# Optimization experiments

Measured on AMD Instinct MI355X. Metric: run time of the kernel, lower is better.

Reference implementation:

```python
import jax, jax.numpy as jnp
import numpy as np

B, C, H, W = 4, 2048, 32, 32
HID, A, G = 512, 9, 20
SCALE = 32.0
POS_T, NEG_T = 0.7, 0.3
W_CONF, W_REG = 1.0, 5.0
EPS = 1e-8


def _anchor_base():
    # gen_anc_centers + gen_anc_base: centers at (i+0.5); anc_w=scale, anc_h=scale*ratio; clipped to feature-map extent
    scales = jnp.array([2.0, 4.0, 6.0])
    ratios = jnp.array([0.5, 1.0, 1.5])
    aw = jnp.repeat(scales, 3)                       # [A]
    ah = (scales[:, None] * ratios[None, :]).reshape(-1)
    xc = (jnp.arange(W) + 0.5)[None, :, None]        # [1,W,1]
    yc = (jnp.arange(H) + 0.5)[:, None, None]        # [H,1,1]
    x1 = jnp.clip(xc - aw / 2, 0.0, W)
    y1 = jnp.clip(yc - ah / 2, 0.0, H)
    x2 = jnp.clip(xc + aw / 2, 0.0, W)
    y2 = jnp.clip(yc + ah / 2, 0.0, H)
    anc = jnp.stack(jnp.broadcast_arrays(x1, y1, x2, y2), axis=-1)  # [H,W,A,4]
    return anc.reshape(-1, 4)                        # [N,4], N = H*W*A


def _conv(x, w, b):
    y = jax.lax.conv_general_dilated(x, w, (1, 1), 'SAME',
                                     dimension_numbers=('NCHW', 'OIHW', 'NCHW'))
    return y + b[None, :, None, None]


def setup_inputs():
    key = jax.random.key(0)
    ks = jax.random.split(key, 8)
    feature_map = jax.random.normal(ks[0], (B, C, H, W), jnp.float32)
    # valid GT boxes in pixel coords of a 1024x1024 image
    ctr = jax.random.uniform(ks[1], (B, G, 2), minval=0.15, maxval=0.85) * 1024.0
    wh = jax.random.uniform(ks[2], (B, G, 2), minval=0.05, maxval=0.30) * 1024.0
    gt_bboxes = jnp.clip(jnp.concatenate([ctr - wh / 2, ctr + wh / 2], -1), 0.0, 1024.0)
    gt_classes = jax.random.randint(ks[3], (B, G), 1, 21)
    f1 = 1.0 / np.sqrt(C * 9)
    f2 = 1.0 / np.sqrt(HID)
    conv1_w = jax.random.uniform(ks[4], (HID, C, 3, 3), jnp.float32, -f1, f1)
    conv1_b = jnp.zeros((HID,), jnp.float32)
    conf_w = jax.random.uniform(ks[5], (A, HID, 1, 1), jnp.float32, -f2, f2)
    conf_b = jnp.zeros((A,), jnp.float32)
    reg_w = jax.random.uniform(ks[6], (A * 4, HID, 1, 1), jnp.float32, -f2, f2)
    reg_b = jnp.zeros((A * 4,), jnp.float32)
    return {"feature_map": feature_map, "gt_bboxes": gt_bboxes, "gt_classes": gt_classes,
            "conv1_w": conv1_w, "conv1_b": conv1_b, "conf_w": conf_w, "conf_b": conf_b,
            "reg_w": reg_w, "reg_b": reg_b}


def reference(feature_map, gt_bboxes, gt_classes, conv1_w, conv1_b, conf_w, conf_b, reg_w, reg_b):
    # ProposalModule (dropout = eval identity)
    hid = jax.nn.relu(_conv(feature_map, conv1_w, conv1_b))
    conf = _conv(hid, conf_w, conf_b).transpose(0, 2, 3, 1).reshape(B, -1)       # [B,N]
    offs = _conv(hid, reg_w, reg_b).transpose(0, 2, 3, 1).reshape(B, -1, 4)      # [B,N,4]

    anc = _anchor_base()                              # [N,4]
    gt = gt_bboxes / SCALE                            # project_bboxes p2a

    # IoU [B,N,G]
    lt = jnp.maximum(anc[None, :, None, :2], gt[:, None, :, :2])
    rb = jnp.minimum(anc[None, :, None, 2:], gt[:, None, :, 2:])
    inter = jnp.clip(rb - lt, 0.0).prod(-1)
    area_a = (anc[:, 2] - anc[:, 0]) * (anc[:, 3] - anc[:, 1])
    area_g = (gt[..., 2] - gt[..., 0]) * (gt[..., 3] - gt[..., 1])
    iou = inter / (area_a[None, :, None] + area_g[:, None, :] - inter + EPS)

    # positive: IoU > pos_thresh OR best anchor for each GT; negative: max IoU < neg_thresh
    max_per_gt = iou.max(axis=1, keepdims=True)
    pos = ((iou > POS_T) | ((iou == max_per_gt) & (max_per_gt > EPS))).any(-1)    # [B,N]
    max_per_anc = iou.max(-1)
    gi = iou.argmax(-1)                               # assigned GT per anchor
    neg = (max_per_anc < NEG_T) & (~pos)

    assigned = jnp.take_along_axis(gt, jnp.broadcast_to(gi[:, :, None], gi.shape + (4,)), axis=1)

    acx = (anc[:, 0] + anc[:, 2]) / 2; acy = (anc[:, 1] + anc[:, 3]) / 2
    aw_ = anc[:, 2] - anc[:, 0];       ah_ = anc[:, 3] - anc[:, 1]
    gcx = (assigned[..., 0] + assigned[..., 2]) / 2; gcy = (assigned[..., 1] + assigned[..., 3]) / 2
    gw = assigned[..., 2] - assigned[..., 0];        gh = assigned[..., 3] - assigned[..., 1]
    gt_off = jnp.stack([(gcx - acx) / (aw_ + EPS), (gcy - acy) / (ah_ + EPS),
                        jnp.log((gw + EPS) / (aw_ + EPS)), jnp.log((gh + EPS) / (ah_ + EPS))], -1)

    posf = pos.astype(conf.dtype)
    negf = neg.astype(conf.dtype)
    # BCE-with-logits, reduction='sum' / batch_size (pos target 1, neg target 0)
    cls_loss = ((jax.nn.softplus(-conf) * posf).sum() + (jax.nn.softplus(conf) * negf).sum()) / B
    d = offs - gt_off
    sl1 = jnp.where(jnp.abs(d) < 1.0, 0.5 * d * d, jnp.abs(d) - 0.5)
    reg_loss = (sl1 * posf[..., None]).sum() / B
    total = W_CONF * cls_loss + W_REG * reg_loss

    # generate_proposals from positive anchors + predicted offsets (mask instead of gather for jit)
    pcx = acx + offs[..., 0] * aw_; pcy = acy + offs[..., 1] * ah_
    pw = aw_ * jnp.exp(offs[..., 2]); ph = ah_ * jnp.exp(offs[..., 3])
    proposals = jnp.stack([pcx - pw / 2, pcy - ph / 2, pcx + pw / 2, pcy + ph / 2], -1)
    proposals = proposals * posf[..., None]
    return total, proposals, pos
```

## Files before the change

### kernel.cpp

```cpp
#include <hip/hip_runtime.h>


typedef __bf16 bf16x8 __attribute__((ext_vector_type(8)));
typedef float floatx4 __attribute__((ext_vector_type(4)));

#define NB 4
#define NC 2048
#define NH 32
#define NW 32
#define NHID 512
#define NA 9
#define NG 20
#define NANC 9216
#define NM 4096

#define OFF_XH    0ull
#define OFF_WT    18939904ull
#define OFF_WH    37814272ull
#define OFF_HB    37863424ull
#define OFF_MAXG  37863680ull
#define OFF_SUMS  37864192ull
#define OFF_CTR   37864320ull
#define OFF_HIDP  37864448ull

#define PREP_TX   4096
#define PREP_W    1024
#define PREP_WH   96
#define PREP_HALO 528
#define PREP_MAXG 80
#define PREP_NBLK (PREP_TX + PREP_W + PREP_WH + PREP_HALO + PREP_MAXG + 1)

__device__ __forceinline__ unsigned short f2bf(float f) {
  unsigned int u = __float_as_uint(f);
  u = (u + 0x7fffu + ((u >> 16) & 1u)) >> 16;
  return (unsigned short)u;
}

__device__ __forceinline__ void gload16(const void* g, void* l) {
  __builtin_amdgcn_global_load_lds(
      (const __attribute__((address_space(1))) unsigned int*)g,
      (__attribute__((address_space(3))) unsigned int*)l, 16, 0, 0);
}

__constant__ float c_aw[9] = {2.f,2.f,2.f,4.f,4.f,4.f,6.f,6.f,6.f};
__constant__ float c_ah[9] = {1.f,2.f,3.f,2.f,4.f,6.f,3.f,6.f,9.f};

struct Anc { float x1, y1, x2, y2, areaA; };
__device__ __forceinline__ Anc anc_of(int n) {
  const int a = n % 9, pix = n / 9;
  const int xi = pix & 31, yi = pix >> 5;
  const float hw = c_aw[a]*0.5f, hh = c_ah[a]*0.5f;
  const float xc = xi + 0.5f, yc = yi + 0.5f;
  Anc A;
  A.x1 = fminf(fmaxf(xc - hw, 0.f), 32.f);
  A.y1 = fminf(fmaxf(yc - hh, 0.f), 32.f);
  A.x2 = fminf(fmaxf(xc + hw, 0.f), 32.f);
  A.y2 = fminf(fmaxf(yc + hh, 0.f), 32.f);
  A.areaA = __fmul_rn(__fsub_rn(A.x2, A.x1), __fsub_rn(A.y2, A.y1));
  return A;
}
__device__ __forceinline__ float iou_one(const Anc& A, float4 gp) {
  const float gx1 = gp.x * 0.03125f, gy1 = gp.y * 0.03125f;
  const float gx2 = gp.z * 0.03125f, gy2 = gp.w * 0.03125f;
  const float dx = fmaxf(__fsub_rn(fminf(A.x2, gx2), fmaxf(A.x1, gx1)), 0.f);
  const float dy = fmaxf(__fsub_rn(fminf(A.y2, gy2), fmaxf(A.y1, gy1)), 0.f);
  const float inter = __fmul_rn(dx, dy);
  const float areaG = __fmul_rn(__fsub_rn(gx2, gx1), __fsub_rn(gy2, gy1));
  const float den = __fadd_rn(__fsub_rn(__fadd_rn(A.areaA, areaG), inter), 1e-8f);
  return __fdiv_rn(inter, den);
}

__global__ __launch_bounds__(256) void k_prep(const float* __restrict__ x,
                                              const float* __restrict__ w1,
                                              const float* __restrict__ cw, const float* __restrict__ cb,
                                              const float* __restrict__ rw, const float* __restrict__ rb,
                                              const float* __restrict__ gtb,
                                              unsigned short* __restrict__ xh,
                                              unsigned short* __restrict__ wt,
                                              unsigned short* __restrict__ wh, float* __restrict__ hb,
                                              unsigned int* __restrict__ maxg,
                                              float* __restrict__ sums, unsigned int* __restrict__ ctr) {
  __shared__ float tile[64][33];
  __shared__ unsigned short wlds[9*1024];
  __shared__ float red[4];
  const int bid = blockIdx.x;
  const int tid = threadIdx.x;

  if (bid < PREP_TX) {
    const int c0 = (bid & 31) << 6;
    const int h  = (bid >> 5) & 31;
    const int b  = bid >> 10;
    const float* src = x + (((size_t)b*NC + c0)*NH + h)*NW;
    const int w4 = (tid & 7) << 2, cl = tid >> 3;
#pragma unroll
    for (int j = 0; j < 2; ++j) {
      const int c = cl + j*32;
      const float4 v = *(const float4*)(src + (size_t)c*NH*NW + w4);
      tile[c][w4 + 0] = v.x;
      tile[c][w4 + 1] = v.y;
      tile[c][w4 + 2] = v.z;
      tile[c][w4 + 3] = v.w;
    }
    __syncthreads();
    unsigned short* dst = xh + ((size_t)(b*34 + h + 1)*34 + 1)*2048 + c0;
    const int w2 = tid >> 3, c8 = (tid & 7) << 3;
    unsigned int pk[4];
#pragma unroll
    for (int k = 0; k < 4; ++k) {
      const unsigned int lo = f2bf(tile[c8 + 2*k][w2]);
      const unsigned int hi = f2bf(tile[c8 + 2*k + 1][w2]);
      pk[k] = lo | (hi << 16);
    }
    *(uint4*)(dst + (size_t)w2*2048 + c8) = make_uint4(pk[0], pk[1], pk[2], pk[3]);
    return;
  }
  if (bid < PREP_TX + PREP_W) {
    const int p = bid - PREP_TX;
    const int o = p >> 1, half = p & 1;
    const int c_base = half << 10;
    const float* src = w1 + ((size_t)(o*2048 + c_base))*9;
#pragma unroll
    for (int j = 0; j < 9; ++j) {
      const int f0 = (j*256 + tid)*4;
      const float4 v = *(const float4*)(src + f0);
      const float vv[4] = {v.x, v.y, v.z, v.w};
#pragma unroll
      for (int e = 0; e < 4; ++e) {
        const int f = f0 + e;
        const int c = f/9, g = f - c*9;
        wlds[g*1024 + c] = f2bf(vv[e]);
      }
    }
    __syncthreads();
#pragma unroll
    for (int j = 0; j < 5; ++j) {
      const int idx = j*256 + tid;
      if (idx < 1152) {
        const int g = idx >> 7, off = (idx & 127) << 3;
        *(uint4*)(wt + (size_t)g*NHID*NC + o*2048 + c_base + off) =
            *(const uint4*)(wlds + g*1024 + off);
      }
    }
    return;
  }
  if (bid < PREP_TX + PREP_W + PREP_WH) {
    const int t = (bid - PREP_TX - PREP_W)*256 + tid;
    const int n = t >> 9, c = t & 511;
    float v = 0.f;
    if (n < 9) v = cw[n*512 + c];
    else if (n < 45) v = rw[(n-9)*512 + c];
    wh[t] = f2bf(v);
    if (c == 0) {
      float bv = 0.f;
      if (n < 9) bv = cb[n];
      else if (n < 45) bv = rb[n-9];
      hb[n] = bv;
    }
    return;
  }
  if (bid < PREP_TX + PREP_W + PREP_WH + PREP_HALO) {
    const int q = bid - (PREP_TX + PREP_W + PREP_WH);
    const int b = q / 132, hc = q - b*132;
    int hh, ww;
    if (hc < 34)       { hh = 0;        ww = hc; }
    else if (hc < 68)  { hh = 33;       ww = hc - 34; }
    else if (hc < 100) { hh = hc - 67;  ww = 0; }
    else               { hh = hc - 99;  ww = 33; }
    uint4* dst = (uint4*)(xh + ((size_t)((b*34 + hh)*34 + ww))*2048);
    dst[tid] = make_uint4(0u, 0u, 0u, 0u);
    return;
  }
  if (bid < PREP_TX + PREP_W + PREP_WH + PREP_HALO + PREP_MAXG) {
    const int p = bid - (PREP_TX + PREP_W + PREP_WH + PREP_HALO);
    const int b = p / NG, g = p - b*NG;
    const float4 gp = *(const float4*)(gtb + ((size_t)b*NG + g)*4);
    float m = 0.f;
#pragma unroll
    for (int j = 0; j < 36; ++j)
      m = fmaxf(m, iou_one(anc_of(tid + j*256), gp));
#pragma unroll
    for (int o = 32; o > 0; o >>= 1) m = fmaxf(m, __shfl_xor(m, o));
    if ((tid & 63) == 0) red[tid >> 6] = m;
    __syncthreads();
    if (tid == 0)
      maxg[b*NG + g] = __float_as_uint(fmaxf(fmaxf(red[0], red[1]), fmaxf(red[2], red[3])));
    return;
  }
  if (tid < 2) sums[tid] = 0.f;
  else if (tid == 2) *ctr = 0u;
}

__global__ __launch_bounds__(256, 4) void k_conv_gemm(const unsigned short* __restrict__ xh,
                                                      const unsigned short* __restrict__ wt,
                                                      unsigned short* __restrict__ hidp,
                                                      int csplit, int ksh) {
  __shared__ unsigned short As[128*64] __attribute__((aligned(16)));
  __shared__ unsigned short Bs[128*64] __attribute__((aligned(16)));
  const int t = threadIdx.x;
  const int L = blockIdx.x;
  const int kz = L & ((1 << ksh) - 1);
  const int rem = L >> ksh;
  const int tileM = rem & 31, tileN = rem >> 5;
  const int b = tileM >> 3, h0 = (tileM & 7) << 2;
  const int o0 = tileN << 7;
  const int wv = t >> 6, lane = t & 63;
  const int wm = wv >> 1, wn = wv & 1;
  const int quad = lane >> 4, l16 = lane & 15;
  const int c_base = kz * csplit;

  floatx4 acc[4][4];
#pragma unroll
  for (int mt = 0; mt < 4; ++mt)
#pragma unroll
    for (int nt = 0; nt < 4; ++nt)
      acc[mt][nt] = (floatx4){0.f, 0.f, 0.f, 0.f};

  const int lr = lane >> 3, pos = lane & 7;
  int gA[4], gB[4];
#pragma unroll
  for (int j = 0; j < 4; ++j) {
    const int row = wv*32 + j*8 + lr;
    const int sd = (pos - row) & 7;
    const int hh = h0 + (row >> 5) + 1, ww = (row & 31) + 1;
    gA[j] = ((b*34 + hh)*34 + ww)*2048 + c_base + sd*8;
    gB[j] = (o0 + row)*2048 + c_base + sd*8;
  }

  for (int g = 0; g < 9; ++g) {
    const int dsp = ((g/3 - 1)*34 + (g%3 - 1)) * 2048;
    const unsigned short* wgp = wt + (size_t)g*NHID*NC;
    for (int c0 = 0; c0 < csplit; c0 += 64) {
#pragma unroll
      for (int j = 0; j < 4; ++j) {
        gload16(xh + gA[j] + dsp + c0, As + (wv*32 + j*8)*64);
        gload16(wgp + gB[j] + c0,      Bs + (wv*32 + j*8)*64);
      }
      __syncthreads();
#pragma unroll
      for (int sub = 0; sub < 2; ++sub) {
        const int ps = ((sub*4 + quad) + l16) & 7;
        bf16x8 af[4], bw[4];
#pragma unroll
        for (int mt = 0; mt < 4; ++mt)
          af[mt] = *(const bf16x8*)(As + (wm*64 + mt*16 + l16)*64 + ps*8);
#pragma unroll
        for (int nt = 0; nt < 4; ++nt)
          bw[nt] = *(const bf16x8*)(Bs + (wn*64 + nt*16 + l16)*64 + ps*8);
#pragma unroll
        for (int mt = 0; mt < 4; ++mt)
#pragma unroll
          for (int nt = 0; nt < 4; ++nt)
            acc[mt][nt] = __builtin_amdgcn_mfma_f32_16x16x32_bf16(af[mt], bw[nt], acc[mt][nt], 0, 0, 0);
      }
      __syncthreads();
    }
  }
  unsigned short* hp = hidp + (size_t)kz*NM*NHID;
#pragma unroll
  for (int mt = 0; mt < 4; ++mt) {
    const int m = tileM*128 + wm*64 + mt*16 + quad*4;
#pragma unroll
    for (int nt = 0; nt < 4; ++nt) {
      const int o = o0 + wn*64 + nt*16 + l16;
#pragma unroll
      for (int r = 0; r < 4; ++r)
        hp[(size_t)(m + r)*NHID + o] = f2bf(acc[mt][nt][r]);
    }
  }
}

__device__ __forceinline__ float softplusf(float z) {
  return fmaxf(z, 0.f) + log1pf(expf(-fabsf(z)));
}
__device__ __forceinline__ float sl1f(float d) {
  const float ad = fabsf(d);
  return ad < 1.f ? 0.5f*d*d : ad - 0.5f;
}

__global__ __launch_bounds__(256) void k_heads_assign(const unsigned short* __restrict__ hidp,
                                                      const float* __restrict__ b1,
                                                      const unsigned short* __restrict__ wh,
                                                      const float* __restrict__ hb,
                                                      const float* __restrict__ gtb,
                                                      const unsigned int* __restrict__ maxg,
                                                      float* __restrict__ out,
                                                      float* __restrict__ sums,
                                                      unsigned int* __restrict__ ctr,
                                                      int nsplit) {
  __shared__ float red[4][16][48];
  __shared__ float hl[16][49];
  __shared__ float4 gt_s[20];
  __shared__ float  mg_s[20];
  const int t = threadIdx.x;
  const int bid = blockIdx.x;
  const int b = bid >> 6, pix0 = (bid & 63) << 4;

  if (t < 20) {
    gt_s[t] = *(const float4*)(gtb + ((size_t)b*NG + t)*4);
    mg_s[t] = __uint_as_float(maxg[b*NG + t]);
  }

  const int wv = t >> 6, lane = t & 63;
  const int quad = lane >> 4, l16 = lane & 15;
  floatx4 acc[3];
#pragma unroll
  for (int nt = 0; nt < 3; ++nt) acc[nt] = (floatx4){0.f, 0.f, 0.f, 0.f};

  const int m = bid*16 + l16;
#pragma unroll
  for (int kk = 0; kk < 4; ++kk) {
    const int ch0 = wv*128 + kk*32 + quad*8;
    float s[8] = {0.f,0.f,0.f,0.f,0.f,0.f,0.f,0.f};
    const unsigned short* hp0 = hidp + (size_t)m*NHID + ch0;
#define SP_ACC(SP) do { \
      const uint4 v = *(const uint4*)(hp0 + (size_t)(SP)*NM*NHID); \
      s[0] += __uint_as_float(v.x << 16); s[1] += __uint_as_float(v.x & 0xffff0000u); \
      s[2] += __uint_as_float(v.y << 16); s[3] += __uint_as_float(v.y & 0xffff0000u); \
      s[4] += __uint_as_float(v.z << 16); s[5] += __uint_as_float(v.z & 0xffff0000u); \
      s[6] += __uint_as_float(v.w << 16); s[7] += __uint_as_float(v.w & 0xffff0000u); \
    } while (0)
    if (nsplit == 8) {
#pragma unroll
      for (int sp = 0; sp < 8; ++sp) SP_ACC(sp);
    } else if (nsplit == 4) {
#pragma unroll
      for (int sp = 0; sp < 4; ++sp) SP_ACC(sp);
    } else {
      for (int sp = 0; sp < nsplit; ++sp) SP_ACC(sp);
    }
#undef SP_ACC
    union { unsigned short u[8]; bf16x8 v; } af;
#pragma unroll
    for (int e = 0; e < 8; ++e)
      af.u[e] = f2bf(fmaxf(s[e] + b1[ch0 + e], 0.f));
#pragma unroll
    for (int nt = 0; nt < 3; ++nt) {
      const bf16x8 bf = *(const bf16x8*)(wh + (size_t)(nt*16 + l16)*NHID + ch0);
      acc[nt] = __builtin_amdgcn_mfma_f32_16x16x32_bf16(af.v, bf, acc[nt], 0, 0, 0);
    }
  }
#pragma unroll
  for (int nt = 0; nt < 3; ++nt)
#pragma unroll
    for (int r = 0; r < 4; ++r)
      red[wv][quad*4 + r][nt*16 + l16] = acc[nt][r];
  __syncthreads();
#pragma unroll
  for (int j = 0; j < 3; ++j) {
    const int idx = t + j*256;
    const int i = idx / 48, c = idx - i*48;
    hl[i][c] = red[0][i][c] + red[1][i][c] + red[2][i][c] + red[3][i][c] + hb[c];
  }
  __syncthreads();

  float cs = 0.f, rs = 0.f;
  if (t < 144) {
    const int pixL = t / 9, a = t - pixL*9;
    const int pix = pix0 + pixL;
    const int n = pix*9 + a;
    const int idx = b*NANC + n;
    const Anc A = anc_of(n);

    float mx = -1.f; int gi = 0; bool pos = false;
    for (int g = 0; g < NG; ++g) {
      const float v = iou_one(A, gt_s[g]);
      const float mg = mg_s[g];
      pos = pos || (v > 0.7f) || ((v == mg) && (mg > 1e-8f));
      if (v > mx) { mx = v; gi = g; }
    }
    const bool neg = (mx < 0.3f) && !pos;
    const float posf = pos ? 1.f : 0.f;

    const float conf = hl[pixL][a];
    const float of0 = hl[pixL][9 + a*4 + 0];
    const float of1 = hl[pixL][9 + a*4 + 1];
    const float of2 = hl[pixL][9 + a*4 + 2];
    const float of3 = hl[pixL][9 + a*4 + 3];

    if (pos) cs = softplusf(-conf);
    else if (neg) cs = softplusf(conf);

    const float acx = (A.x1 + A.x2)*0.5f, acy = (A.y1 + A.y2)*0.5f;
    const float aw = A.x2 - A.x1, ah = A.y2 - A.y1;
    if (pos) {
      const float4 gp = gt_s[gi];
      const float gx1 = gp.x*0.03125f, gy1 = gp.y*0.03125f;
      const float gx2 = gp.z*0.03125f, gy2 = gp.w*0.03125f;
      const float gcx = (gx1+gx2)*0.5f, gcy = (gy1+gy2)*0.5f;
      const float gw = gx2-gx1, gh = gy2-gy1;
      const float t0 = (gcx-acx)/(aw+1e-8f), t1 = (gcy-acy)/(ah+1e-8f);
      const float t2 = logf((gw+1e-8f)/(aw+1e-8f)), t3 = logf((gh+1e-8f)/(ah+1e-8f));
      rs = sl1f(of0-t0) + sl1f(of1-t1) + sl1f(of2-t2) + sl1f(of3-t3);
    }

    const float pcx = acx + of0*aw, pcy = acy + of1*ah;
    const float pw = aw*expf(of2), ph = ah*expf(of3);
    float* op = out + 1 + (size_t)idx*4;
    op[0] = (pcx - pw*0.5f)*posf;
    op[1] = (pcy - ph*0.5f)*posf;
    op[2] = (pcx + pw*0.5f)*posf;
    op[3] = (pcy + ph*0.5f)*posf;
    out[1 + 4*(size_t)NB*NANC + idx] = posf;
  }
#pragma unroll
  for (int o = 32; o > 0; o >>= 1) { cs += __shfl_xor(cs, o); rs += __shfl_xor(rs, o); }
  if ((t & 63) == 0) { atomicAdd(&sums[0], cs); atomicAdd(&sums[1], rs); }

  __syncthreads();
  if (t == 0) {
    __threadfence();
    const unsigned int c = atomicAdd(ctr, 1u);
    if (c == 255u) {
      __threadfence();
      const float fcs = atomicAdd(&sums[0], 0.f);
      const float frs = atomicAdd(&sums[1], 0.f);
      out[0] = fcs*0.25f + 5.f*(frs*0.25f);
    }
  }
}

extern "C" void kernel_launch(void* const* d_in, const int* in_sizes, int n_in,
                              void* d_out, int out_size, void* d_ws, size_t ws_size,
                              hipStream_t stream) {
  const float* x   = (const float*)d_in[0];
  const float* gtb = (const float*)d_in[1];
  const float* w1  = (const float*)d_in[3];
  const float* b1  = (const float*)d_in[4];
  const float* cw  = (const float*)d_in[5];
  const float* cb  = (const float*)d_in[6];
  const float* rw  = (const float*)d_in[7];
  const float* rb  = (const float*)d_in[8];
  float* out = (float*)d_out;
  char* ws = (char*)d_ws;

  unsigned short* xh    = (unsigned short*)(ws + OFF_XH);
  unsigned short* wt    = (unsigned short*)(ws + OFF_WT);
  unsigned short* wh    = (unsigned short*)(ws + OFF_WH);
  float*          hb    = (float*)(ws + OFF_HB);
  unsigned int*   maxg  = (unsigned int*)(ws + OFF_MAXG);
  float*          sums  = (float*)(ws + OFF_SUMS);
  unsigned int*   ctr   = (unsigned int*)(ws + OFF_CTR);
  unsigned short* hidp  = (unsigned short*)(ws + OFF_HIDP);

  int nsplit = 8, ksh = 3;
  while (nsplit > 1 && OFF_HIDP + (size_t)nsplit*NM*NHID*2 > ws_size) { nsplit >>= 1; --ksh; }
  const int csplit = NC / nsplit;

  k_prep<<<PREP_NBLK, 256, 0, stream>>>(x, w1, cw, cb, rw, rb, gtb, xh, wt, wh, hb, maxg, sums, ctr);
  k_conv_gemm<<<128*nsplit, 256, 0, stream>>>(xh, wt, hidp, csplit, ksh);
  k_heads_assign<<<256, 256, 0, stream>>>(hidp, b1, wh, hb, gtb, maxg, out, sums, ctr, nsplit);
}
```

Baseline: 225.8 us.

## Pre-swizzle conv weights into MFMA fragment order and load B directly to registers

The weight prep kernel now writes the 3x3 conv weights in a layout matching the MFMA B-fragment order, so each lane in the GEMM loads its bf16x8 fragments straight from global memory. This removes the Bs shared-memory tile and its LDS writes and reads, which frees LDS and may raise occupancy. The cost is that weight tiles shared across blocks are no longer staged through LDS, so each wave issues its own global/L2 loads. Those loads now sit in the K-loop before the barrier.

Result: slower. 250.6 us (+11.0%).

```diff
diff --git a/kernel.cpp b/kernel.cpp
--- a/kernel.cpp
+++ b/kernel.cpp
@@ -118,6 +118,7 @@
     const int p = bid - PREP_TX;
     const int o = p >> 1, half = p & 1;
     const int c_base = half << 10;
+    const int og = o >> 4, l16o = o & 15;
     const float* src = w1 + ((size_t)(o*2048 + c_base))*9;
 #pragma unroll
     for (int j = 0; j < 9; ++j) {
@@ -136,9 +137,12 @@
     for (int j = 0; j < 5; ++j) {
       const int idx = j*256 + tid;
       if (idx < 1152) {
-        const int g = idx >> 7, off = (idx & 127) << 3;
-        *(uint4*)(wt + (size_t)g*NHID*NC + o*2048 + c_base + off) =
-            *(const uint4*)(wlds + g*1024 + off);
+        const int g = idx >> 7, r = idx & 127;
+        const int cq_loc = r >> 3, s = (r >> 2) & 1, quad = r & 3;
+        const int cqg = (half << 4) + cq_loc;
+        const size_t dst = ((size_t)((g*32 + cqg)*2 + s))*16384
+                         + (size_t)((og*4 + quad)*128 + l16o*8);
+        *(uint4*)(wt + dst) = *(const uint4*)(wlds + g*1024 + cq_loc*64 + (s*4 + quad)*8);
       }
     }
     return;
@@ -195,7 +199,6 @@
                                                       unsigned short* __restrict__ hidp,
                                                       int csplit, int ksh) {
   __shared__ unsigned short As[128*64] __attribute__((aligned(16)));
-  __shared__ unsigned short Bs[128*64] __attribute__((aligned(16)));
   const int t = threadIdx.x;
   const int L = blockIdx.x;
   const int kz = L & ((1 << ksh) - 1);
@@ -216,41 +219,44 @@
       acc[mt][nt] = (floatx4){0.f, 0.f, 0.f, 0.f};
 
   const int lr = lane >> 3, pos = lane & 7;
-  int gA[4], gB[4];
+  int gA[4];
 #pragma unroll
   for (int j = 0; j < 4; ++j) {
     const int row = wv*32 + j*8 + lr;
     const int sd = (pos - row) & 7;
     const int hh = h0 + (row >> 5) + 1, ww = (row & 31) + 1;
     gA[j] = ((b*34 + hh)*34 + ww)*2048 + c_base + sd*8;
-    gB[j] = (o0 + row)*2048 + c_base + sd*8;
-  }
+  }
+
+  const unsigned short* wB = wt + (size_t)(tileN*8 + wn*4)*512 + (size_t)lane*8;
 
   for (int g = 0; g < 9; ++g) {
     const int dsp = ((g/3 - 1)*34 + (g%3 - 1)) * 2048;
-    const unsigned short* wgp = wt + (size_t)g*NHID*NC;
     for (int c0 = 0; c0 < csplit; c0 += 64) {
-#pragma unroll
-      for (int j = 0; j < 4; ++j) {
+      const int cqg = (c_base + c0) >> 6;
+      const unsigned short* wBk = wB + ((size_t)((g*32 + cqg)*2))*16384;
+#pragma unroll
+      for (int j = 0; j < 4; ++j)
         gload16(xh + gA[j] + dsp + c0, As + (wv*32 + j*8)*64);
-        gload16(wgp + gB[j] + c0,      Bs + (wv*32 + j*8)*64);
-      }
+      bf16x8 bw[2][4];
+#pragma unroll
+      for (int s = 0; s < 2; ++s)
+#pragma unroll
+        for (int nt = 0; nt < 4; ++nt)
+          bw[s][nt] = *(const bf16x8*)(wBk + (size_t)s*16384 + nt*512);
       __syncthreads();
 #pragma unroll
       for (int sub = 0; sub < 2; ++sub) {
         const int ps = ((sub*4 + quad) + l16) & 7;
-        bf16x8 af[4], bw[4];
+        bf16x8 af[4];
 #pragma unroll
         for (int mt = 0; mt < 4; ++mt)
           af[mt] = *(const bf16x8*)(As + (wm*64 + mt*16 + l16)*64 + ps*8);
 #pragma unroll
-        for (int nt = 0; nt < 4; ++nt)
-          bw[nt] = *(const bf16x8*)(Bs + (wn*64 + nt*16 + l16)*64 + ps*8);
-#pragma unroll
         for (int mt = 0; mt < 4; ++mt)
 #pragma unroll
           for (int nt = 0; nt < 4; ++nt)
-            acc[mt][nt] = __builtin_amdgcn_mfma_f32_16x16x32_bf16(af[mt], bw[nt], acc[mt][nt], 0, 0, 0);
+            acc[mt][nt] = __builtin_amdgcn_mfma_f32_16x16x32_bf16(af[mt], bw[sub][nt], acc[mt][nt], 0, 0, 0);
       }
       __syncthreads();
     }
```
